# Kernel optimization log

Measured on AMD Instinct MI355X. Metric: run time of the kernel, lower is better.

Reference implementation:

```python
import jax, jax.numpy as jnp
import numpy as np

B, ORDER, S, D, H = 64, 2, 256, 256, 8
HD = D // H  # head_dim = 32


def setup_inputs() -> dict:
    key = jax.random.key(0)
    ks = jax.random.split(key, 6)
    stdv = 1.0 / np.sqrt(HD)
    return {
        "x": jax.random.normal(ks[0], (B, ORDER, S, D), jnp.float32),
        "A": jax.random.randint(ks[1], (B, ORDER, S, S), 0, 5, jnp.int32),
        # params stacked as [order, conv(1|2), ...]
        "Wp": jax.random.normal(ks[2], (ORDER, 2, D, D), jnp.float32) * stdv,
        "bp": jnp.zeros((ORDER, 2, D), jnp.float32),
        "att_src": jax.random.normal(ks[3], (ORDER, 2, H, HD), jnp.float32) * stdv,
        "att_dst": jax.random.normal(ks[4], (ORDER, 2, H, HD), jnp.float32) * stdv,
        "gbias": jnp.zeros((ORDER, 2, D), jnp.float32),
        "prelu_a": 0.25 * jnp.ones((D,), jnp.float32),
    }


def _gat(x, edge, W, b, a_src, a_dst, gb):
    """Dense additive GAT over a [B,S,S] boolean adjacency. Eval mode (dropout inert)."""
    Bt, St, Dt = x.shape
    x = x @ W + b                                   # project (bias=True)
    xh = x.reshape(Bt, St, H, HD)
    a_s = jnp.einsum('bshd,hd->bsh', xh, a_src)     # per-source score
    a_d = jnp.einsum('bthd,hd->bth', xh, a_dst)     # per-dest score
    alpha = a_s[:, :, None, :] + a_d[:, None, :, :]  # [B, S_src, S_dst, H]
    alpha = jnp.where(edge[..., None], alpha, 0.0)   # masked_fill((A != 1), 0)
    alpha = jnp.where(alpha >= 0, alpha, 0.2 * alpha)  # leaky_relu(0.2)
    alpha = jax.nn.softmax(alpha, axis=1)            # stable softmax over source axis
    out = jnp.einsum('bsth,bshd->bthd', alpha, xh).reshape(Bt, St, Dt)
    return out + x + gb                              # add_self_loops + bias


def reference(x, A, Wp, bp, att_src, att_dst, gbias, prelu_a):
    # A1 = (A==2)+(A==4); A2 = (A==3)+(A==4); edge iff value == 1
    A1 = (A == 2) | (A == 4)
    A2 = (A == 3) | (A == 4)
    hs = []
    for i in range(ORDER):  # order is a small structural constant (=2)
        h1 = _gat(x[:, i], A1[:, i], Wp[i, 0], bp[i, 0], att_src[i, 0], att_dst[i, 0], gbias[i, 0])
        h2 = _gat(x[:, i], A2[:, i], Wp[i, 1], bp[i, 1], att_src[i, 1], att_dst[i, 1], gbias[i, 1])
        hs.append(h1 + h2)
    h = jnp.stack(hs, axis=1)                       # [B, order, S, D]
    out = h + h.mean(axis=1, keepdims=True)
    out = jnp.where(out >= 0, out, prelu_a * out)   # PReLU(dim)
    return out
```

## Files before the change

kernel.cpp:

```cpp
#include <hip/hip_runtime.h>
#include <hip/hip_bf16.h>
#include <math.h>

typedef __bf16 bf16;
typedef __bf16 bf16x4 __attribute__((ext_vector_type(4)));
typedef __bf16 bf16x8 __attribute__((ext_vector_type(8)));
typedef float f32x4 __attribute__((ext_vector_type(4)));
typedef unsigned int u32;

#define LOG2E 1.44269504f

__device__ inline float fast_exp2(float x) {
#if __has_builtin(__builtin_amdgcn_exp2f)
    return __builtin_amdgcn_exp2f(x);
#else
    return exp2f(x);
#endif
}

#define GL2LDS(gp, lp) __builtin_amdgcn_global_load_lds( \
    (const __attribute__((address_space(1))) u32*)(gp),  \
    (__attribute__((address_space(3))) u32*)(lp), 16, 0, 0)


__global__ void prep_k(const float* __restrict__ x, const float* __restrict__ Wp,
                       const int* __restrict__ A, bf16* __restrict__ xb,
                       bf16* __restrict__ Wt, unsigned* __restrict__ m1,
                       unsigned* __restrict__ m2) {
    int bid = blockIdx.x;
    int tid = threadIdx.x;
    if (bid < 4096) {
        int gid = bid * 256 + tid;
        const f32x4* xp = (const f32x4*)x + (size_t)gid * 2;
        f32x4 a = xp[0], b4 = xp[1];
        bf16x8 o;
#pragma unroll
        for (int c = 0; c < 4; ++c) { o[c] = (bf16)a[c]; o[c + 4] = (bf16)b4[c]; }
        ((bf16x8*)xb)[gid] = o;
    } else if (bid < 5120) {
        int gid = (bid - 4096) * 256 + tid;
        int k = gid & 255;
        int n = (gid >> 8) & 255;
        int ij = gid >> 16;
        Wt[gid] = (bf16)Wp[(ij * 256 + k) * 256 + n];
    } else {
        int pb = bid - 5120;
        int sh = pb & 1;
        int ijb = pb >> 1;
        const int* Ab = A + ((size_t)ijb << 16);
        unsigned w1 = 0, w2 = 0;
#pragma unroll 8
        for (int sl = 0; sl < 128; ++sl) {
            int s = sh * 128 + sl;
            int av = Ab[s * 256 + tid];
            unsigned f1 = (av == 2 || av == 4) ? 1u : 0u;
            unsigned f2 = (av == 3 || av == 4) ? 1u : 0u;
            w1 |= f1 << (s & 31);
            w2 |= f2 << (s & 31);
            if ((s & 31) == 31) {
                int kc = s >> 5;
                m1[(ijb * 8 + kc) * 256 + tid] = w1;
                m2[(ijb * 8 + kc) * 256 + tid] = w2;
                w1 = 0; w2 = 0;
            }
        }
    }
}

__launch_bounds__(256)
__global__ void proj_gemm(const bf16* __restrict__ xb, const bf16* __restrict__ Wt,
                          const float* __restrict__ bp, bf16* __restrict__ xpb) {
    __shared__ bf16 As[128 * 32];
    __shared__ bf16 Bs[128 * 32];

    int tid = threadIdx.x;
    int mt = blockIdx.x, nt = blockIdx.y, i = blockIdx.z;
    int n0 = nt * 128;
    int j  = n0 >> 8;
    int d0 = n0 & 255;
    int m0 = mt * 128;

    int c0 = tid, c1 = tid + 256;
    int r0 = c0 >> 2, k80 = (c0 & 3) * 8;
    int r1 = c1 >> 2, k81 = (c1 & 3) * 8;
    int gm0 = m0 + r0, gm1 = m0 + r1;
    const bf16* ga0 = xb + (((size_t)((gm0 >> 8) * 2 + i) * 256 + (gm0 & 255)) << 8) + k80;
    const bf16* ga1 = xb + (((size_t)((gm1 >> 8) * 2 + i) * 256 + (gm1 & 255)) << 8) + k81;
    const bf16* gb0 = Wt + (((size_t)(i * 2 + j) * 256 + d0 + r0) << 8) + k80;
    const bf16* gb1 = Wt + (((size_t)(i * 2 + j) * 256 + d0 + r1) << 8) + k81;
    bf16* la0 = As + c0 * 8;
    bf16* la1 = As + c1 * 8;
    bf16* lb0 = Bs + c0 * 8;
    bf16* lb1 = Bs + c1 * 8;

    int wave = tid >> 6, lane = tid & 63;
    int wm = (wave & 1) * 64, wn = (wave >> 1) * 64;
    int lrow = lane & 15, quad = lane >> 4;

    f32x4 acc[4][4];
#pragma unroll
    for (int a = 0; a < 4; ++a)
#pragma unroll
        for (int c = 0; c < 4; ++c) acc[a][c] = (f32x4){0.f, 0.f, 0.f, 0.f};

    for (int kc = 0; kc < 8; ++kc) {
        int k0 = kc * 32;
        GL2LDS(ga0 + k0, la0);
        GL2LDS(ga1 + k0, la1);
        GL2LDS(gb0 + k0, lb0);
        GL2LDS(gb1 + k0, lb1);
        __syncthreads();
        bf16x8 af[4], bfr[4];
#pragma unroll
        for (int mi = 0; mi < 4; ++mi)
            af[mi] = *(const bf16x8*)&As[(wm + mi * 16 + lrow) * 32 + quad * 8];
#pragma unroll
        for (int ni = 0; ni < 4; ++ni)
            bfr[ni] = *(const bf16x8*)&Bs[(wn + ni * 16 + lrow) * 32 + quad * 8];
#pragma unroll
        for (int mi = 0; mi < 4; ++mi)
#pragma unroll
            for (int ni = 0; ni < 4; ++ni)
                acc[mi][ni] = __builtin_amdgcn_mfma_f32_16x16x32_bf16(af[mi], bfr[ni], acc[mi][ni], 0, 0, 0);
        __syncthreads();
    }

#pragma unroll
    for (int mi = 0; mi < 4; ++mi) {
#pragma unroll
        for (int r = 0; r < 4; ++r) {
            int rowm = m0 + wm + mi * 16 + quad * 4 + r;
            int bb = rowm >> 8, ss = rowm & 255;
            size_t obase = (((size_t)(i * 2 + j) * 64 + bb) * 256 + ss) << 8;
#pragma unroll
            for (int ni = 0; ni < 4; ++ni) {
                int dcol = d0 + wn + ni * 16 + lrow;
                float v = acc[mi][ni][r] + bp[(i * 2 + j) * 256 + dcol];
                xpb[obase + dcol] = (bf16)v;
            }
        }
    }
}

__global__ void score_k(const bf16* __restrict__ xpb, const float* __restrict__ att_src,
                        const float* __restrict__ att_dst, float* __restrict__ asb,
                        float* __restrict__ adb, bf16* __restrict__ Vt) {
    int gid = blockIdx.x * 256 + threadIdx.x;
    int h = gid & 7;
    int r = gid >> 3;
    int s = r & 255;
    int bij = r >> 8;
    int ij = bij >> 6;
    const bf16* row = xpb + ((size_t)r << 8) + h * 32;
    const float* asrc = att_src + (ij * 8 + h) * 32;
    const float* adst = att_dst + (ij * 8 + h) * 32;
    bf16* vout = Vt + (((size_t)(bij * 8 + h)) << 13) + s;
    float ssum = 0.f, dsum = 0.f;
#pragma unroll
    for (int c = 0; c < 4; ++c) {
        bf16x8 v = *(const bf16x8*)(row + c * 8);
#pragma unroll
        for (int q = 0; q < 8; ++q) {
            float f = (float)v[q];
            ssum += f * asrc[c * 8 + q];
            dsum += f * adst[c * 8 + q];
        }
#pragma unroll
        for (int q = 0; q < 8; ++q) vout[(c * 8 + q) << 8] = v[q];
    }
    int oidx = (bij * 8 + h) * 256 + s;
    asb[oidx] = ssum * LOG2E;
    adb[oidx] = dsum * LOG2E;
}

__launch_bounds__(256, 3)
__global__ void attn_k(const bf16* __restrict__ Vt, const unsigned* __restrict__ m1,
                       const unsigned* __restrict__ m2, const float* __restrict__ asb,
                       const float* __restrict__ adb, const float* __restrict__ gbias,
                       float* __restrict__ out) {
    int bid = blockIdx.x;
    int tt = bid & 3, hg = (bid >> 2) & 1, i = (bid >> 3) & 1, b = bid >> 4;
    int t0 = tt * 64;
    int tid = threadIdx.x, wave = tid >> 6, lane = tid & 63;
    int lrow = lane & 15, quad = lane >> 4;
    int h = hg * 4 + wave;

    __shared__ float    as_l[2][4][256];
    __shared__ unsigned ml[2][8][64];
    __shared__ float    l_lds[2][4][64];

#pragma unroll
    for (int p = 0; p < 8; ++p) {
        int c = p >> 2, w = p & 3;
        as_l[c][w][tid] = asb[(((i * 2 + c) * 64 + b) * 8 + hg * 4 + w) * 256 + tid];
    }
    {
        const unsigned* mp0 = m1 + ((b * 2 + i) * 8) * 256 + t0;
        const unsigned* mp1 = m2 + ((b * 2 + i) * 8) * 256 + t0;
#pragma unroll
        for (int p = 0; p < 4; ++p) {
            int idx = p * 256 + tid;
            int c = idx >> 9, kc = (idx >> 6) & 7, tl = idx & 63;
            ml[c][kc][tl] = (c == 0 ? mp0 : mp1)[kc * 256 + tl];
        }
    }
    float ad_r[2][4];
#pragma unroll
    for (int c = 0; c < 2; ++c)
#pragma unroll
        for (int mi = 0; mi < 4; ++mi)
            ad_r[c][mi] = adb[(((i * 2 + c) * 64 + b) * 8 + h) * 256 + t0 + mi * 16 + lrow];
    __syncthreads();

    const bf16* vt0 = Vt + (((size_t)(((i * 2 + 0) * 64 + b) * 8 + h)) << 13);
    const bf16* vt1 = Vt + (((size_t)(((i * 2 + 1) * 64 + b) * 8 + h)) << 13);

    f32x4 acc[2][4][2];
#pragma unroll
    for (int c = 0; c < 2; ++c)
#pragma unroll
        for (int mi = 0; mi < 4; ++mi)
#pragma unroll
            for (int ni = 0; ni < 2; ++ni) acc[c][mi][ni] = (f32x4){0.f, 0.f, 0.f, 0.f};
    float lsum[2][4] = {{0.f, 0.f, 0.f, 0.f}, {0.f, 0.f, 0.f, 0.f}};

    for (int kc = 0; kc < 8; ++kc) {
        int s0 = kc * 32;
        bf16x8 bfr[2][2];
#pragma unroll
        for (int ni = 0; ni < 2; ++ni) {
            bfr[0][ni] = *(const bf16x8*)(vt0 + (size_t)(ni * 16 + lrow) * 256 + s0 + quad * 8);
            bfr[1][ni] = *(const bf16x8*)(vt1 + (size_t)(ni * 16 + lrow) * 256 + s0 + quad * 8);
        }
#pragma unroll
        for (int c = 0; c < 2; ++c) {
            float asv[8];
#pragma unroll
            for (int j = 0; j < 8; ++j) asv[j] = as_l[c][wave][s0 + quad * 8 + j];
#pragma unroll
            for (int mi = 0; mi < 4; ++mi) {
                unsigned w = ml[c][kc][mi * 16 + lrow];
                float ad = ad_r[c][mi];
                bf16x8 af;
#pragma unroll
                for (int j = 0; j < 8; ++j) {
                    float u = asv[j] + ad;
                    u = fmaxf(u, 0.2f * u);
                    u = fminf(u, 115.f);
                    float e = fast_exp2(u);
                    e = ((w >> (quad * 8 + j)) & 1u) ? e : 1.0f;
                    lsum[c][mi] += e;
                    af[j] = (bf16)e;
                }
                acc[c][mi][0] = __builtin_amdgcn_mfma_f32_16x16x32_bf16(af, bfr[c][0], acc[c][mi][0], 0, 0, 0);
                acc[c][mi][1] = __builtin_amdgcn_mfma_f32_16x16x32_bf16(af, bfr[c][1], acc[c][mi][1], 0, 0, 0);
            }
        }
    }

#pragma unroll
    for (int c = 0; c < 2; ++c)
#pragma unroll
        for (int mi = 0; mi < 4; ++mi) {
            float l = lsum[c][mi];
            l += __shfl_xor(l, 16, 64);
            l += __shfl_xor(l, 32, 64);
            if (lane < 16) l_lds[c][wave][mi * 16 + lane] = l;
        }
    __syncthreads();

#pragma unroll
    for (int ni = 0; ni < 2; ++ni) {
        int dcol = h * 32 + ni * 16 + lrow;
        float gb = gbias[(i * 2 + 0) * 256 + dcol] + gbias[(i * 2 + 1) * 256 + dcol];
        const bf16* r0 = vt0 + (size_t)(ni * 16 + lrow) * 256 + t0;
        const bf16* r1 = vt1 + (size_t)(ni * 16 + lrow) * 256 + t0;
#pragma unroll
        for (int mi = 0; mi < 4; ++mi) {
            bf16x4 rv0 = *(const bf16x4*)(r0 + mi * 16 + quad * 4);
            bf16x4 rv1 = *(const bf16x4*)(r1 + mi * 16 + quad * 4);
#pragma unroll
            for (int r = 0; r < 4; ++r) {
                int tl = mi * 16 + quad * 4 + r;
                int t = t0 + tl;
                float inv1 = __builtin_amdgcn_rcpf(l_lds[0][wave][tl]);
                float inv2 = __builtin_amdgcn_rcpf(l_lds[1][wave][tl]);
                float res = (float)rv0[r] + (float)rv1[r];
                float v = acc[0][mi][ni][r] * inv1 + acc[1][mi][ni][r] * inv2 + res + gb;
                out[(((size_t)((b * 2 + i) * 256 + t)) << 8) + dcol] = v;
            }
        }
    }
}

__global__ void final_k(float* __restrict__ out, const float* __restrict__ prelu_a) {
    int gid = blockIdx.x * 256 + threadIdx.x;
    int d4 = gid & 63;
    int s  = (gid >> 6) & 255;
    int b  = gid >> 14;
    f32x4* o = (f32x4*)out;
    size_t i0 = (((size_t)(b * 2 + 0) * 256 + s) << 6) + d4;
    size_t i1 = (((size_t)(b * 2 + 1) * 256 + s) << 6) + d4;
    f32x4 h0 = o[i0], h1 = o[i1];
    f32x4 pa = *(const f32x4*)(prelu_a + d4 * 4);
    f32x4 v0, v1;
#pragma unroll
    for (int c = 0; c < 4; ++c) {
        float mn = 0.5f * (h0[c] + h1[c]);
        float a0 = h0[c] + mn;
        float a1 = h1[c] + mn;
        v0[c] = a0 >= 0.f ? a0 : pa[c] * a0;
        v1[c] = a1 >= 0.f ? a1 : pa[c] * a1;
    }
    o[i0] = v0;
    o[i1] = v1;
}

extern "C" void kernel_launch(void* const* d_in, const int* in_sizes, int n_in,
                              void* d_out, int out_size, void* d_ws, size_t ws_size,
                              hipStream_t stream) {
    const float* x       = (const float*)d_in[0];
    const int*   A       = (const int*)d_in[1];
    const float* Wp      = (const float*)d_in[2];
    const float* bp      = (const float*)d_in[3];
    const float* att_src = (const float*)d_in[4];
    const float* att_dst = (const float*)d_in[5];
    const float* gbias   = (const float*)d_in[6];
    const float* prelu_a = (const float*)d_in[7];
    float* out = (float*)d_out;

    char* ws = (char*)d_ws;
    bf16*     Wt  = (bf16*)ws;
    bf16*     xpb = (bf16*)(ws + 524288);
    float*    asb = (float*)(ws + 34078720);
    float*    adb = (float*)(ws + 36175872);
    unsigned* m1  = (unsigned*)(ws + 38273024);
    unsigned* m2  = (unsigned*)(ws + 39321600);
    bf16*     xbvt = (bf16*)(ws + 40370176);

    prep_k<<<5376, 256, 0, stream>>>(x, Wp, A, xbvt, Wt, m1, m2);
    dim3 gproj(128, 4, 2);
    proj_gemm<<<gproj, 256, 0, stream>>>(xbvt, Wt, bp, xpb);
    score_k<<<2048, 256, 0, stream>>>(xpb, att_src, att_dst, asb, adb, xbvt);
    attn_k<<<1024, 256, 0, stream>>>(xbvt, m1, m2, asb, adb, gbias, out);
    final_k<<<4096, 256, 0, stream>>>(out, prelu_a);
}
```

Before: 234.4 us.

## Fuse attention-score computation and V transpose into projection GEMM epilogue

The projection GEMM now computes W^T·x so its accumulators come out in a feature-major layout. It stages the biased result in LDS, writes the transposed V tensor directly, and computes the per-head source and destination attention scores in the epilogue. This removes the separate score kernel and the round trip of the projected activations through global memory. The attention inner loop also zeroes the masked logit before the exp instead of selecting 1.0 afterwards, and drops the clamp at 115. Dropping the clamp risks overflow for large logits, and the larger LDS footprint may lower GEMM occupancy.

```diff
diff --git a/kernel.cpp b/kernel.cpp
--- a/kernel.cpp
+++ b/kernel.cpp
@@ -69,32 +69,43 @@
 
 __launch_bounds__(256)
 __global__ void proj_gemm(const bf16* __restrict__ xb, const bf16* __restrict__ Wt,
-                          const float* __restrict__ bp, bf16* __restrict__ xpb) {
-    __shared__ bf16 As[128 * 32];
-    __shared__ bf16 Bs[128 * 32];
+                          const float* __restrict__ bp, const float* __restrict__ att_src,
+                          const float* __restrict__ att_dst, bf16* __restrict__ Vt,
+                          float* __restrict__ asb, float* __restrict__ adb) {
+    __shared__ char smem[35840 + 1024];
+    bf16* As = (bf16*)smem;
+    bf16* Bs = (bf16*)(smem + 8192);
+    bf16* TL = (bf16*)smem;
+    float* attL = (float*)(smem + 35840);
 
     int tid = threadIdx.x;
     int mt = blockIdx.x, nt = blockIdx.y, i = blockIdx.z;
     int n0 = nt * 128;
-    int j  = n0 >> 8;
-    int d0 = n0 & 255;
+    int j = n0 >> 8, d0 = n0 & 255;
+    int ij = i * 2 + j;
     int m0 = mt * 128;
+    int b = m0 >> 8, shalf = (m0 >> 7) & 1;
+
+    {
+        int which = tid >> 7, rest = tid & 127;
+        const float* ap = which ? att_dst : att_src;
+        attL[tid] = ap[(ij * 8 + (d0 >> 5) + (rest >> 5)) * 32 + (rest & 31)];
+    }
 
     int c0 = tid, c1 = tid + 256;
     int r0 = c0 >> 2, k80 = (c0 & 3) * 8;
     int r1 = c1 >> 2, k81 = (c1 & 3) * 8;
-    int gm0 = m0 + r0, gm1 = m0 + r1;
-    const bf16* ga0 = xb + (((size_t)((gm0 >> 8) * 2 + i) * 256 + (gm0 & 255)) << 8) + k80;
-    const bf16* ga1 = xb + (((size_t)((gm1 >> 8) * 2 + i) * 256 + (gm1 & 255)) << 8) + k81;
-    const bf16* gb0 = Wt + (((size_t)(i * 2 + j) * 256 + d0 + r0) << 8) + k80;
-    const bf16* gb1 = Wt + (((size_t)(i * 2 + j) * 256 + d0 + r1) << 8) + k81;
+    const bf16* ga0 = xb + (((size_t)((b * 2 + i) * 256 + shalf * 128 + r0)) << 8) + k80;
+    const bf16* ga1 = xb + (((size_t)((b * 2 + i) * 256 + shalf * 128 + r1)) << 8) + k81;
+    const bf16* gb0 = Wt + (((size_t)(ij * 256 + d0 + r0)) << 8) + k80;
+    const bf16* gb1 = Wt + (((size_t)(ij * 256 + d0 + r1)) << 8) + k81;
     bf16* la0 = As + c0 * 8;
     bf16* la1 = As + c1 * 8;
     bf16* lb0 = Bs + c0 * 8;
     bf16* lb1 = Bs + c1 * 8;
 
     int wave = tid >> 6, lane = tid & 63;
-    int wm = (wave & 1) * 64, wn = (wave >> 1) * 64;
+    int wd = (wave & 1) * 64, ws = (wave >> 1) * 64;
     int lrow = lane & 15, quad = lane >> 4;
 
     f32x4 acc[4][4];
@@ -110,67 +121,58 @@
         GL2LDS(gb0 + k0, lb0);
         GL2LDS(gb1 + k0, lb1);
         __syncthreads();
-        bf16x8 af[4], bfr[4];
-#pragma unroll
-        for (int mi = 0; mi < 4; ++mi)
-            af[mi] = *(const bf16x8*)&As[(wm + mi * 16 + lrow) * 32 + quad * 8];
-#pragma unroll
-        for (int ni = 0; ni < 4; ++ni)
-            bfr[ni] = *(const bf16x8*)&Bs[(wn + ni * 16 + lrow) * 32 + quad * 8];
-#pragma unroll
-        for (int mi = 0; mi < 4; ++mi)
-#pragma unroll
-            for (int ni = 0; ni < 4; ++ni)
-                acc[mi][ni] = __builtin_amdgcn_mfma_f32_16x16x32_bf16(af[mi], bfr[ni], acc[mi][ni], 0, 0, 0);
+        bf16x8 wf[4], xf[4];
+#pragma unroll
+        for (int dj = 0; dj < 4; ++dj)
+            wf[dj] = *(const bf16x8*)&Bs[(wd + dj * 16 + lrow) * 32 + quad * 8];
+#pragma unroll
+        for (int sj = 0; sj < 4; ++sj)
+            xf[sj] = *(const bf16x8*)&As[(ws + sj * 16 + lrow) * 32 + quad * 8];
+#pragma unroll
+        for (int dj = 0; dj < 4; ++dj)
+#pragma unroll
+            for (int sj = 0; sj < 4; ++sj)
+                acc[dj][sj] = __builtin_amdgcn_mfma_f32_16x16x32_bf16(wf[dj], xf[sj], acc[dj][sj], 0, 0, 0);
         __syncthreads();
     }
 
 #pragma unroll
-    for (int mi = 0; mi < 4; ++mi) {
+    for (int dj = 0; dj < 4; ++dj) {
 #pragma unroll
         for (int r = 0; r < 4; ++r) {
-            int rowm = m0 + wm + mi * 16 + quad * 4 + r;
-            int bb = rowm >> 8, ss = rowm & 255;
-            size_t obase = (((size_t)(i * 2 + j) * 64 + bb) * 256 + ss) << 8;
-#pragma unroll
-            for (int ni = 0; ni < 4; ++ni) {
-                int dcol = d0 + wn + ni * 16 + lrow;
-                float v = acc[mi][ni][r] + bp[(i * 2 + j) * 256 + dcol];
-                xpb[obase + dcol] = (bf16)v;
-            }
-        }
-    }
-}
-
-__global__ void score_k(const bf16* __restrict__ xpb, const float* __restrict__ att_src,
-                        const float* __restrict__ att_dst, float* __restrict__ asb,
-                        float* __restrict__ adb, bf16* __restrict__ Vt) {
-    int gid = blockIdx.x * 256 + threadIdx.x;
-    int h = gid & 7;
-    int r = gid >> 3;
-    int s = r & 255;
-    int bij = r >> 8;
-    int ij = bij >> 6;
-    const bf16* row = xpb + ((size_t)r << 8) + h * 32;
-    const float* asrc = att_src + (ij * 8 + h) * 32;
-    const float* adst = att_dst + (ij * 8 + h) * 32;
-    bf16* vout = Vt + (((size_t)(bij * 8 + h)) << 13) + s;
-    float ssum = 0.f, dsum = 0.f;
-#pragma unroll
-    for (int c = 0; c < 4; ++c) {
-        bf16x8 v = *(const bf16x8*)(row + c * 8);
-#pragma unroll
-        for (int q = 0; q < 8; ++q) {
-            float f = (float)v[q];
-            ssum += f * asrc[c * 8 + q];
-            dsum += f * adst[c * 8 + q];
-        }
-#pragma unroll
-        for (int q = 0; q < 8; ++q) vout[(c * 8 + q) << 8] = v[q];
-    }
-    int oidx = (bij * 8 + h) * 256 + s;
-    asb[oidx] = ssum * LOG2E;
-    adb[oidx] = dsum * LOG2E;
+            int dl = wd + dj * 16 + quad * 4 + r;
+            float bias = bp[ij * 256 + d0 + dl];
+#pragma unroll
+            for (int sj = 0; sj < 4; ++sj)
+                TL[dl * 140 + ws + sj * 16 + lrow] = (bf16)(acc[dj][sj][r] + bias);
+        }
+    }
+    __syncthreads();
+
+    {
+        int dl = tid >> 1, sh64 = (tid & 1) * 64;
+        const bf16* src = TL + dl * 140 + sh64;
+        bf16* dst = Vt + (((size_t)(ij * 64 + b)) << 16) + (size_t)(d0 + dl) * 256
+                    + shalf * 128 + sh64;
+#pragma unroll
+        for (int q = 0; q < 16; ++q)
+            *(bf16x4*)(dst + q * 4) = *(const bf16x4*)(src + q * 4);
+    }
+
+    {
+        int s = tid & 127, which = tid >> 7;
+        const float* av = attL + which * 128;
+        float* outp = which ? adb : asb;
+#pragma unroll
+        for (int hl = 0; hl < 4; ++hl) {
+            float accs = 0.f;
+#pragma unroll
+            for (int d = 0; d < 32; ++d)
+                accs += (float)TL[(hl * 32 + d) * 140 + s] * av[hl * 32 + d];
+            int hg = (d0 >> 5) + hl;
+            outp[((ij * 64 + b) * 8 + hg) * 256 + shalf * 128 + s] = accs * LOG2E;
+        }
+    }
 }
 
 __launch_bounds__(256, 3)
@@ -239,16 +241,15 @@
             for (int j = 0; j < 8; ++j) asv[j] = as_l[c][wave][s0 + quad * 8 + j];
 #pragma unroll
             for (int mi = 0; mi < 4; ++mi) {
-                unsigned w = ml[c][kc][mi * 16 + lrow];
+                unsigned wb = ml[c][kc][mi * 16 + lrow] >> (quad * 8);
                 float ad = ad_r[c][mi];
                 bf16x8 af;
 #pragma unroll
                 for (int j = 0; j < 8; ++j) {
                     float u = asv[j] + ad;
                     u = fmaxf(u, 0.2f * u);
-                    u = fminf(u, 115.f);
+                    u = ((wb >> j) & 1u) ? u : 0.f;
                     float e = fast_exp2(u);
-                    e = ((w >> (quad * 8 + j)) & 1u) ? e : 1.0f;
                     lsum[c][mi] += e;
                     af[j] = (bf16)e;
                 }
@@ -331,17 +332,16 @@
 
     char* ws = (char*)d_ws;
     bf16*     Wt  = (bf16*)ws;
-    bf16*     xpb = (bf16*)(ws + 524288);
-    float*    asb = (float*)(ws + 34078720);
-    float*    adb = (float*)(ws + 36175872);
-    unsigned* m1  = (unsigned*)(ws + 38273024);
-    unsigned* m2  = (unsigned*)(ws + 39321600);
-    bf16*     xbvt = (bf16*)(ws + 40370176);
-
-    prep_k<<<5376, 256, 0, stream>>>(x, Wp, A, xbvt, Wt, m1, m2);
+    unsigned* m1  = (unsigned*)(ws + 524288);
+    unsigned* m2  = (unsigned*)(ws + 1572864);
+    float*    asb = (float*)(ws + 2621440);
+    float*    adb = (float*)(ws + 4718592);
+    bf16*     xb  = (bf16*)(ws + 6815744);
+    bf16*     Vt  = (bf16*)(ws + 23592960);
+
+    prep_k<<<5376, 256, 0, stream>>>(x, Wp, A, xb, Wt, m1, m2);
     dim3 gproj(128, 4, 2);
-    proj_gemm<<<gproj, 256, 0, stream>>>(xbvt, Wt, bp, xpb);
-    score_k<<<2048, 256, 0, stream>>>(xpb, att_src, att_dst, asb, adb, xbvt);
-    attn_k<<<1024, 256, 0, stream>>>(xbvt, m1, m2, asb, adb, gbias, out);
+    proj_gemm<<<gproj, 256, 0, stream>>>(xb, Wt, bp, att_src, att_dst, Vt, asb, adb);
+    attn_k<<<1024, 256, 0, stream>>>(Vt, m1, m2, asb, adb, gbias, out);
     final_k<<<4096, 256, 0, stream>>>(out, prelu_a);
 }
```

New measurement: 210.4 us. 1.11x faster.
